# Optimization experiments

Measured on AMD Instinct MI355X. Metric: run time of the kernel, lower is better.

The kernel has to match this reference:

```python
import jax, jax.numpy as jnp
import numpy as np

# Model config (matches init_kwargs)
DIM = 2048
INTER = 1408          # moe_inter_dim
E = 16                # n_routed_experts
TOPK = 4              # n_activated_experts
G = 4                 # n_expert_groups
TOPK_G = 2            # n_limited_groups
N_SHARED = 2
SHARED_INTER = N_SHARED * INTER  # 2816
ROUTE_SCALE = 1.0


def setup_inputs() -> dict:
    key = jax.random.key(0)
    ks = jax.random.split(key, 8)
    s = 0.02
    x = jax.random.normal(ks[0], (1, 2048, DIM), dtype=jnp.float32)
    Wg = jax.random.normal(ks[1], (E, DIM), dtype=jnp.float32) * s      # gate weight
    W1 = jax.random.normal(ks[2], (E, INTER, DIM), dtype=jnp.float32) * s  # expert gate proj
    W3 = jax.random.normal(ks[3], (E, INTER, DIM), dtype=jnp.float32) * s  # expert up proj
    W2 = jax.random.normal(ks[4], (E, DIM, INTER), dtype=jnp.float32) * s  # expert down proj
    Ws1 = jax.random.normal(ks[5], (SHARED_INTER, DIM), dtype=jnp.float32) * s
    Ws3 = jax.random.normal(ks[6], (SHARED_INTER, DIM), dtype=jnp.float32) * s
    Ws2 = jax.random.normal(ks[7], (DIM, SHARED_INTER), dtype=jnp.float32) * s
    return {"x": x, "Wg": Wg, "W1": W1, "W3": W3, "W2": W2,
            "Ws1": Ws1, "Ws3": Ws3, "Ws2": Ws2}


def _moe_forward(x, Wg, W1, W3, W2, Ws1, Ws3, Ws2):
    B, S, D = x.shape
    xt = x.reshape(-1, D)              # [T, D]
    T = xt.shape[0]

    # ---- Gate: group-limited top-k routing (bias is None since dim != 7168) ----
    scores = jax.nn.softmax(xt @ Wg.T, axis=-1)          # [T, E]
    sg = scores.reshape(T, G, E // G)                    # [T, G, E/G]
    group_scores = sg.max(axis=-1)                       # amax per group
    gidx = jax.lax.top_k(group_scores, TOPK_G)[1]        # [T, TOPK_G]
    gmask = jax.nn.one_hot(gidx, G, dtype=jnp.float32).sum(axis=1) > 0  # [T, G] kept groups
    masked = jnp.where(gmask[:, :, None], sg, -jnp.inf).reshape(T, E)
    topi = jax.lax.top_k(masked, TOPK)[1]                # [T, TOPK] expert indices
    weights = jnp.take_along_axis(scores, topi, axis=1) * ROUTE_SCALE  # original_scores gather

    # ---- Routed experts: dense per-expert SwiGLU FFN, zero-weight combine ----
    # combine[t, e] = sum over k of weights[t, k] * (topi[t, k] == e)
    combine = jnp.zeros((T, E), xt.dtype).at[jnp.arange(T)[:, None], topi].add(weights)
    h = jax.nn.silu(jnp.einsum('td,eid->eti', xt, W1)) * jnp.einsum('td,eid->eti', xt, W3)
    expert_out = jnp.einsum('eti,edi->etd', h, W2)       # [E, T, D]
    y = jnp.einsum('etd,te->td', expert_out, combine)    # [T, D]

    # ---- Shared expert (applied to all tokens) ----
    z = (jax.nn.silu(xt @ Ws1.T) * (xt @ Ws3.T)) @ Ws2.T

    return (y + z).reshape(B, S, D)


def reference(x, Wg, W1, W3, W2, Ws1, Ws3, Ws2):
    return _moe_forward(x, Wg, W1, W3, W2, Ws1, Ws3, Ws2)
```

## Files before the change

kernel.cpp:

```cpp
#include <hip/hip_runtime.h>
#include <stdint.h>

#define D_MODEL  2048
#define N_INTER  1408
#define SH_INTER 2816
#define T_TOK    2048
#define NSLOT    (T_TOK * 4)
#define MIB(x)   ((size_t)(x) << 20)

typedef __attribute__((ext_vector_type(8))) short bf16x8;
typedef __attribute__((ext_vector_type(4))) float f32x4;

__device__ __forceinline__ unsigned short f2bf(float f){
  unsigned int b = __builtin_bit_cast(unsigned int, f);
  b = (b + 0x7FFFu + ((b >> 16) & 1u)) >> 16;
  return (unsigned short)b;
}
__device__ __forceinline__ float bf2f(unsigned short h){
  unsigned int b = ((unsigned int)h) << 16;
  return __builtin_bit_cast(float, b);
}

#define GLOAD16(gp, lp) __builtin_amdgcn_global_load_lds( \
    (const __attribute__((address_space(1))) unsigned int*)(gp), \
    (__attribute__((address_space(3))) unsigned int*)(lp), 16, 0, 0)

__global__ void cvt_bf16_kernel(const float* __restrict__ x,
                                unsigned short* __restrict__ o, int n4){
  const int stride = gridDim.x * blockDim.x;
  for (int i = blockIdx.x * blockDim.x + threadIdx.x; i < n4; i += stride){
    const float4 v = ((const float4*)x)[i];
    ushort4 u; u.x = f2bf(v.x); u.y = f2bf(v.y); u.z = f2bf(v.z); u.w = f2bf(v.w);
    ((ushort4*)o)[i] = u;
  }
}

__global__ void gate_kernel(const float* __restrict__ x, const float* __restrict__ Wg,
                            int* __restrict__ cnt, int* __restrict__ list,
                            float* __restrict__ wslot){
  const int t = blockIdx.x;
  const int l = threadIdx.x;
  const int e = l & 15, q = l >> 4;
  const float* xr = x + (size_t)t * D_MODEL + q * 512;
  const float* wr = Wg + (size_t)e * D_MODEL + q * 512;
  float p = 0.f;
  #pragma unroll 4
  for (int i = 0; i < 512; i += 4){
    float4 xv = *(const float4*)(xr + i);
    float4 wv = *(const float4*)(wr + i);
    p += xv.x*wv.x + xv.y*wv.y + xv.z*wv.z + xv.w*wv.w;
  }
  p += __shfl_xor(p, 16);
  p += __shfl_xor(p, 32);
  float mx = p;
  for (int d = 1; d < 16; d <<= 1) mx = fmaxf(mx, __shfl_xor(mx, d));
  float ex = __expf(p - mx);
  float sum = ex;
  for (int d = 1; d < 16; d <<= 1) sum += __shfl_xor(sum, d);
  const float sc = ex / sum;
  float gm = fmaxf(sc, __shfl_xor(sc, 1));
  gm = fmaxf(gm, __shfl_xor(gm, 2));
  const float g0 = __shfl(gm, 0), g1 = __shfl(gm, 4),
              g2 = __shfl(gm, 8), g3 = __shfl(gm, 12);
  const int grp = e >> 2;
  const float gs[4] = {g0, g1, g2, g3};
  int grank = 0;
  #pragma unroll
  for (int j = 0; j < 4; ++j)
    if (gs[j] > gm || (gs[j] == gm && j < grp)) grank++;
  const float msc = (grank < 2) ? sc : -INFINITY;
  int erank = 0;
  #pragma unroll
  for (int j = 0; j < 16; ++j){
    const float oj = __shfl(msc, j);
    if (oj > msc || (oj == msc && j < e)) erank++;
  }
  if (q == 0 && erank < 4 && msc > -INFINITY){
    const int pos = atomicAdd(&cnt[e], 1);
    const int slot = (t << 2) | erank;
    list[e * T_TOK + pos] = slot;
    wslot[slot] = sc;
  }
}

template<int GATHER>
__global__ __launch_bounds__(256, 2)
void gemm_gu2_kernel(const unsigned short* __restrict__ A,
                     const unsigned short* __restrict__ BG,
                     const unsigned short* __restrict__ BU,
                     unsigned short* __restrict__ H,
                     const int* __restrict__ list,
                     const int* __restrict__ cnt,
                     int K, int NI, int MT, int NT)
{
  __shared__ unsigned short As [3 * 4096];
  __shared__ unsigned short BsG[3 * 4096];
  __shared__ unsigned short BsU[3 * 4096];

  const int per = gridDim.x >> 3;
  const int gsw = (blockIdx.x & 7) * per + (blockIdx.x >> 3);
  const int mt   = gsw % MT;
  const int rest = gsw / MT;
  const int nt = GATHER ? (rest % NT) : rest;
  const int e  = GATHER ? (rest / NT) : 0;
  const int cntE = GATHER ? cnt[e] : (MT * 128);
  if (mt * 128 >= cntE) return;

  const int tid = threadIdx.x, wid = tid >> 6, lane = tid & 63;
  const int sx = ((lane & 3) ^ ((lane >> 3) & 3)) << 3;

  const int rt0 = 32 * wid + (lane >> 2), rt1 = rt0 + 16;
  int ar0, ar1;
  if (GATHER){
    const int lim = cntE - 1;
    int p0 = mt * 128 + rt0; p0 = p0 < lim ? p0 : lim;
    int p1 = mt * 128 + rt1; p1 = p1 < lim ? p1 : lim;
    ar0 = list[e * T_TOK + p0] >> 2;
    ar1 = list[e * T_TOK + p1] >> 2;
  } else { ar0 = mt * 128 + rt0; ar1 = mt * 128 + rt1; }
  const unsigned short* pa0 = A + (size_t)ar0 * K + sx;
  const unsigned short* pa1 = A + (size_t)ar1 * K + sx;

  const size_t eoff = GATHER ? (size_t)e * NI * K : 0;
  const unsigned short* pg0 = BG + eoff + (size_t)(nt * 128 + rt0) * K + sx;
  const unsigned short* pg1 = pg0 + (size_t)16 * K;
  const unsigned short* pu0 = BU + eoff + (size_t)(nt * 128 + rt0) * K + sx;
  const unsigned short* pu1 = pu0 + (size_t)16 * K;

  const int w0 = (32 * wid) * 32, w1 = w0 + 512;
  const int bufStr = 4096;

  const int wr = wid >> 1, wc = wid & 1, lr = lane & 15, lq = lane >> 4;
  const int fx = ((lq ^ ((lr >> 1) & 3)) << 3);
  int aoff[4], boff[4];
  #pragma unroll
  for (int m = 0; m < 4; ++m) aoff[m] = (wr * 64 + m * 16 + lr) * 32 + fx;
  #pragma unroll
  for (int n = 0; n < 4; ++n) boff[n] = (wc * 64 + n * 16 + lr) * 32 + fx;

  f32x4 accg[4][4], accu[4][4];
  const f32x4 zero = {0.f, 0.f, 0.f, 0.f};
  #pragma unroll
  for (int m = 0; m < 4; ++m)
    #pragma unroll
    for (int n = 0; n < 4; ++n){ accg[m][n] = zero; accu[m][n] = zero; }

  const int KT = K >> 5;
  #pragma unroll
  for (int t = 0; t < 3; ++t){
    GLOAD16(pa0, As  + t * bufStr + w0);
    GLOAD16(pa1, As  + t * bufStr + w1);
    GLOAD16(pg0, BsG + t * bufStr + w0);
    GLOAD16(pg1, BsG + t * bufStr + w1);
    GLOAD16(pu0, BsU + t * bufStr + w0);
    GLOAD16(pu1, BsU + t * bufStr + w1);
    pa0 += 32; pa1 += 32; pg0 += 32; pg1 += 32; pu0 += 32; pu1 += 32;
  }
  int c = 0;

  for (int kt = 0; kt < KT; ++kt){
    if (kt < KT - 2)       asm volatile("s_waitcnt vmcnt(12)" ::: "memory");
    else if (kt == KT - 2) asm volatile("s_waitcnt vmcnt(6)"  ::: "memory");
    else                   asm volatile("s_waitcnt vmcnt(0)"  ::: "memory");
    __builtin_amdgcn_s_barrier();

    const unsigned short* aC = As  + c * bufStr;
    const unsigned short* gC = BsG + c * bufStr;
    const unsigned short* uC = BsU + c * bufStr;
    bf16x8 af[4], bg[4], bu[4];
    #pragma unroll
    for (int m = 0; m < 4; ++m) af[m] = *(const bf16x8*)(aC + aoff[m]);
    #pragma unroll
    for (int n = 0; n < 4; ++n) bg[n] = *(const bf16x8*)(gC + boff[n]);
    #pragma unroll
    for (int n = 0; n < 4; ++n) bu[n] = *(const bf16x8*)(uC + boff[n]);

    asm volatile("s_waitcnt lgkmcnt(0)" ::: "memory");
    __builtin_amdgcn_sched_barrier(0);
    __builtin_amdgcn_s_barrier();

    if (kt + 3 < KT){
      GLOAD16(pa0, As  + c * bufStr + w0);
      GLOAD16(pa1, As  + c * bufStr + w1);
      GLOAD16(pg0, BsG + c * bufStr + w0);
      GLOAD16(pg1, BsG + c * bufStr + w1);
      GLOAD16(pu0, BsU + c * bufStr + w0);
      GLOAD16(pu1, BsU + c * bufStr + w1);
      pa0 += 32; pa1 += 32; pg0 += 32; pg1 += 32; pu0 += 32; pu1 += 32;
    }

    __builtin_amdgcn_s_setprio(1);
    #pragma unroll
    for (int n = 0; n < 4; ++n)
      #pragma unroll
      for (int m = 0; m < 4; ++m){
        accg[m][n] = __builtin_amdgcn_mfma_f32_16x16x32_bf16(af[m], bg[n], accg[m][n], 0, 0, 0);
        accu[m][n] = __builtin_amdgcn_mfma_f32_16x16x32_bf16(af[m], bu[n], accu[m][n], 0, 0, 0);
      }
    __builtin_amdgcn_s_setprio(0);

    c = (c == 2) ? 0 : c + 1;
  }

  const int colBase = nt * 128 + wc * 64;
  #pragma unroll
  for (int m = 0; m < 4; ++m){
    #pragma unroll
    for (int r = 0; r < 4; ++r){
      const int grow = mt * 128 + wr * 64 + m * 16 + lq * 4 + r;
      if (GATHER && grow >= cntE) continue;
      const int orow = GATHER ? list[e * T_TOK + grow] : grow;
      unsigned short* op = H + (size_t)orow * NI + colBase;
      #pragma unroll
      for (int n = 0; n < 4; ++n){
        const float g = accg[m][n][r], u = accu[m][n][r];
        op[n * 16 + lr] = f2bf(g / (1.f + __expf(-g)) * u);
      }
    }
  }
}

template<int GATHER, int KS>
__global__ __launch_bounds__(256, 2)
void gemm_down_kernel(const unsigned short* __restrict__ A,
                      const unsigned short* __restrict__ B,
                      void* __restrict__ OutP,
                      const int* __restrict__ list,
                      const int* __restrict__ cnt,
                      int K, int N, int MT, int NT)
{
  __shared__ __align__(128) char smem[24576 + 49152];
  unsigned short* As = (unsigned short*)smem;
  unsigned short* Bs = (unsigned short*)(smem + 24576);

  const int per = gridDim.x >> 3;
  const int gsw = (blockIdx.x & 7) * per + (blockIdx.x >> 3);
  const int mt   = gsw % MT;
  int rest = gsw / MT;
  const int nt = rest % NT; rest /= NT;
  const int ks = (KS > 1) ? (rest % KS) : 0;
  const int e  = GATHER ? (rest / (KS > 1 ? KS : 1)) : 0;
  const int cntE = GATHER ? cnt[e] : (MT * 128);
  if (mt * 128 >= cntE) return;

  const int tid = threadIdx.x, wid = tid >> 6, lane = tid & 63;
  const int sx = ((lane & 3) ^ ((lane >> 3) & 3)) << 3;
  const int kOff = ks * (K / KS);

  const int rt0 = 32 * wid + (lane >> 2), rt1 = rt0 + 16;
  int ar0, ar1;
  if (GATHER){
    const int lim = cntE - 1;
    int p0 = mt * 128 + rt0; p0 = p0 < lim ? p0 : lim;
    int p1 = mt * 128 + rt1; p1 = p1 < lim ? p1 : lim;
    ar0 = list[e * T_TOK + p0];
    ar1 = list[e * T_TOK + p1];
  } else { ar0 = mt * 128 + rt0; ar1 = mt * 128 + rt1; }
  const unsigned short* pa0 = A + (size_t)ar0 * K + kOff + sx;
  const unsigned short* pa1 = A + (size_t)ar1 * K + kOff + sx;

  const unsigned short* wsrc = B + (GATHER ? (size_t)e * N * K : 0) + kOff;
  const int rb = 64 * wid + (lane >> 2);
  const unsigned short* pb0 = wsrc + (size_t)(nt * 256 + rb     ) * K + sx;
  const unsigned short* pb1 = wsrc + (size_t)(nt * 256 + rb + 16) * K + sx;
  const unsigned short* pb2 = wsrc + (size_t)(nt * 256 + rb + 32) * K + sx;
  const unsigned short* pb3 = wsrc + (size_t)(nt * 256 + rb + 48) * K + sx;

  const int aW0 = (32 * wid) * 32, aW1 = aW0 + 512;
  const int bW  = (64 * wid) * 32;
  const int aStr = 128 * 32, bStr = 256 * 32;

  const int wr = wid >> 1, wc = wid & 1, lr = lane & 15, lq = lane >> 4;
  const int fx = ((lq ^ ((lr >> 1) & 3)) << 3);
  int aoff[4], boff[8];
  #pragma unroll
  for (int m = 0; m < 4; ++m) aoff[m] = (wr * 64 + m * 16 + lr) * 32 + fx;
  #pragma unroll
  for (int n = 0; n < 8; ++n) boff[n] = (wc * 128 + n * 16 + lr) * 32 + fx;

  f32x4 acc[4][8];
  const f32x4 zero = {0.f, 0.f, 0.f, 0.f};
  #pragma unroll
  for (int m = 0; m < 4; ++m)
    #pragma unroll
    for (int n = 0; n < 8; ++n) acc[m][n] = zero;

  const int KT = (K / KS) >> 5;
  #pragma unroll
  for (int t = 0; t < 3; ++t){
    GLOAD16(pa0, As + t * aStr + aW0);
    GLOAD16(pa1, As + t * aStr + aW1);
    GLOAD16(pb0, Bs + t * bStr + bW);
    GLOAD16(pb1, Bs + t * bStr + bW + 512);
    GLOAD16(pb2, Bs + t * bStr + bW + 1024);
    GLOAD16(pb3, Bs + t * bStr + bW + 1536);
    pa0 += 32; pa1 += 32; pb0 += 32; pb1 += 32; pb2 += 32; pb3 += 32;
  }
  int c = 0;

  for (int kt = 0; kt < KT; ++kt){
    if (kt < KT - 2)       asm volatile("s_waitcnt vmcnt(12)" ::: "memory");
    else if (kt == KT - 2) asm volatile("s_waitcnt vmcnt(6)"  ::: "memory");
    else                   asm volatile("s_waitcnt vmcnt(0)"  ::: "memory");
    __builtin_amdgcn_s_barrier();

    const unsigned short* aC = As + c * aStr;
    const unsigned short* bC = Bs + c * bStr;
    bf16x8 af[4], bf[8];
    #pragma unroll
    for (int m = 0; m < 4; ++m) af[m] = *(const bf16x8*)(aC + aoff[m]);
    #pragma unroll
    for (int n = 0; n < 8; ++n) bf[n] = *(const bf16x8*)(bC + boff[n]);

    asm volatile("s_waitcnt lgkmcnt(0)" ::: "memory");
    __builtin_amdgcn_sched_barrier(0);
    __builtin_amdgcn_s_barrier();

    if (kt + 3 < KT){
      GLOAD16(pa0, As + c * aStr + aW0);
      GLOAD16(pa1, As + c * aStr + aW1);
      GLOAD16(pb0, Bs + c * bStr + bW);
      GLOAD16(pb1, Bs + c * bStr + bW + 512);
      GLOAD16(pb2, Bs + c * bStr + bW + 1024);
      GLOAD16(pb3, Bs + c * bStr + bW + 1536);
      pa0 += 32; pa1 += 32; pb0 += 32; pb1 += 32; pb2 += 32; pb3 += 32;
    }

    __builtin_amdgcn_s_setprio(1);
    #pragma unroll
    for (int n = 0; n < 8; ++n)
      #pragma unroll
      for (int m = 0; m < 4; ++m)
        acc[m][n] = __builtin_amdgcn_mfma_f32_16x16x32_bf16(af[m], bf[n], acc[m][n], 0, 0, 0);
    __builtin_amdgcn_s_setprio(0);

    c = (c == 2) ? 0 : c + 1;
  }

  const int colBase = nt * 256 + wc * 128;
  #pragma unroll
  for (int m = 0; m < 4; ++m){
    #pragma unroll
    for (int r = 0; r < 4; ++r){
      const int grow = mt * 128 + wr * 64 + m * 16 + lq * 4 + r;
      if (GATHER == 0){
        float* op = (float*)OutP + (size_t)ks * MT * 128 * N + (size_t)grow * N + colBase;
        #pragma unroll
        for (int n = 0; n < 8; ++n) op[n * 16 + lr] = acc[m][n][r];
      } else {
        if (grow >= cntE) continue;
        const int orow = list[e * T_TOK + grow];
        unsigned short* op = (unsigned short*)OutP + (size_t)orow * N + colBase;
        #pragma unroll
        for (int n = 0; n < 8; ++n) op[n * 16 + lr] = f2bf(acc[m][n][r]);
      }
    }
  }
}

__global__ void combine_kernel(const unsigned short* __restrict__ H2,
                               const float* __restrict__ P,
                               const float* __restrict__ wslot,
                               float* __restrict__ out){
  const int t = blockIdx.x;
  const int ccol = threadIdx.x * 8;
  float w[4];
  #pragma unroll
  for (int k = 0; k < 4; ++k) w[k] = wslot[t * 4 + k];
  float a[8];
  #pragma unroll
  for (int j = 0; j < 8; ++j) a[j] = 0.f;
  #pragma unroll
  for (int p = 0; p < 4; ++p){
    const float* pp = P + (size_t)(p * T_TOK + t) * D_MODEL + ccol;
    #pragma unroll
    for (int j = 0; j < 8; ++j) a[j] += pp[j];
  }
  #pragma unroll
  for (int k = 0; k < 4; ++k){
    const bf16x8 hv = *(const bf16x8*)(H2 + (size_t)(t * 4 + k) * D_MODEL + ccol);
    #pragma unroll
    for (int j = 0; j < 8; ++j) a[j] += w[k] * bf2f((unsigned short)hv[j]);
  }
  float* o = out + (size_t)t * D_MODEL + ccol;
  #pragma unroll
  for (int j = 0; j < 8; ++j) o[j] = a[j];
}

extern "C" void kernel_launch(void* const* d_in, const int* in_sizes, int n_in,
                              void* d_out, int out_size, void* d_ws, size_t ws_size,
                              hipStream_t stream)
{
  const float* x   = (const float*)d_in[0];
  const float* Wg  = (const float*)d_in[1];
  const float* W1  = (const float*)d_in[2];
  const float* W3  = (const float*)d_in[3];
  const float* W2  = (const float*)d_in[4];
  const float* Ws1 = (const float*)d_in[5];
  const float* Ws3 = (const float*)d_in[6];
  const float* Ws2 = (const float*)d_in[7];
  float* out = (float*)d_out;

  char* ws = (char*)d_ws;
  int*   cnt   = (int*)(ws);
  int*   list  = (int*)(ws + 4096);
  float* wslot = (float*)(ws + 4096 + 131072);
  unsigned short* xbf = (unsigned short*)(ws + MIB(1));
  unsigned short* H2  = (unsigned short*)(ws + MIB(1));
  unsigned short* Hs  = (unsigned short*)(ws + MIB(34));
  unsigned short* Hr  = (unsigned short*)(ws + MIB(46));
  float*          P   = (float*)        (ws + MIB(70));
  unsigned short* WA  = (unsigned short*)(ws + MIB(138));
  unsigned short* WB  = (unsigned short*)(ws + MIB(231));

  hipMemsetAsync(cnt, 0, 4096, stream);
  cvt_bf16_kernel<<<2048, 256, 0, stream>>>(x, xbf, T_TOK * D_MODEL / 4);
  gate_kernel<<<T_TOK, 64, 0, stream>>>(x, Wg, cnt, list, wslot);

  cvt_bf16_kernel<<<2048, 256, 0, stream>>>(Ws1, WA, SH_INTER * D_MODEL / 4);
  cvt_bf16_kernel<<<2048, 256, 0, stream>>>(Ws3, WB, SH_INTER * D_MODEL / 4);
  gemm_gu2_kernel<0><<<16 * 22, 256, 0, stream>>>(xbf, WA, WB, Hs, nullptr, nullptr,
                                                  D_MODEL, SH_INTER, 16, 22);
  cvt_bf16_kernel<<<2048, 256, 0, stream>>>(Ws2, WA, D_MODEL * SH_INTER / 4);
  gemm_down_kernel<0, 4><<<16 * 8 * 4, 256, 0, stream>>>(Hs, WA, P, nullptr, nullptr,
                                                         SH_INTER, D_MODEL, 16, 8);

  cvt_bf16_kernel<<<8192, 256, 0, stream>>>(W1, WA, 16 * N_INTER * D_MODEL / 4);
  cvt_bf16_kernel<<<8192, 256, 0, stream>>>(W3, WB, 16 * N_INTER * D_MODEL / 4);
  gemm_gu2_kernel<1><<<16 * 11 * 16, 256, 0, stream>>>(xbf, WA, WB, Hr, list, cnt,
                                                       D_MODEL, N_INTER, 16, 11);
  cvt_bf16_kernel<<<8192, 256, 0, stream>>>(W2, WA, 16 * D_MODEL * N_INTER / 4);
  gemm_down_kernel<1, 1><<<16 * 8 * 16, 256, 0, stream>>>(Hr, WA, H2, list, cnt,
                                                          N_INTER, D_MODEL, 16, 8);
  combine_kernel<<<T_TOK, 256, 0, stream>>>(H2, P, wslot, out);
}
```

Baseline: 613.1 us.

## Overlap weight bf16 conversion with GEMMs via extra tail blocks

Routed-expert weight conversions (W1, W3, W2) are folded into the preceding GEMM launches as extra blocks, so conversion streams while the GEMM blocks compute. The four small conversions (x and the shared-expert weights) merge into one kernel. The shared down-projection drops its split-K, writes straight into the output, and combine accumulates onto it instead of summing four partial buffers. This cuts launch count and serial conversion time, but the shared down GEMM now launches only 128 GEMM blocks and competes with conversion blocks for bandwidth.

```diff
diff --git a/kernel.cpp b/kernel.cpp
--- a/kernel.cpp
+++ b/kernel.cpp
@@ -25,13 +25,36 @@
     (const __attribute__((address_space(1))) unsigned int*)(gp), \
     (__attribute__((address_space(3))) unsigned int*)(lp), 16, 0, 0)
 
-__global__ void cvt_bf16_kernel(const float* __restrict__ x,
-                                unsigned short* __restrict__ o, int n4){
+__device__ __forceinline__ void cvt_tail(const float* __restrict__ src,
+                                         unsigned short* __restrict__ dst,
+                                         int n4, int cb, int nblk, int tid){
+  const float4* s = (const float4*)src;
+  ushort4* d = (ushort4*)dst;
+  const int stride = nblk * 256;
+  for (int i = cb * 256 + tid; i < n4; i += stride){
+    const float4 v = s[i];
+    ushort4 u; u.x = f2bf(v.x); u.y = f2bf(v.y); u.z = f2bf(v.z); u.w = f2bf(v.w);
+    d[i] = u;
+  }
+}
+
+__global__ void cvt4_kernel(const float* __restrict__ x,  const float* __restrict__ Ws1,
+                            const float* __restrict__ Ws3, const float* __restrict__ Ws2,
+                            unsigned short* __restrict__ xbf, unsigned short* __restrict__ S1,
+                            unsigned short* __restrict__ S3,  unsigned short* __restrict__ S2){
+  const int N0 = T_TOK * D_MODEL / 4;
+  const int NW = SH_INTER * D_MODEL / 4;
+  const int total = N0 + 3 * NW;
   const int stride = gridDim.x * blockDim.x;
-  for (int i = blockIdx.x * blockDim.x + threadIdx.x; i < n4; i += stride){
-    const float4 v = ((const float4*)x)[i];
+  for (int i = blockIdx.x * blockDim.x + threadIdx.x; i < total; i += stride){
+    const float4* s; ushort4* d; int j;
+    if (i < N0)            { s = (const float4*)x;   d = (ushort4*)xbf; j = i; }
+    else if (i < N0 + NW)  { s = (const float4*)Ws1; d = (ushort4*)S1;  j = i - N0; }
+    else if (i < N0 + 2*NW){ s = (const float4*)Ws3; d = (ushort4*)S3;  j = i - N0 - NW; }
+    else                   { s = (const float4*)Ws2; d = (ushort4*)S2;  j = i - N0 - 2*NW; }
+    const float4 v = s[j];
     ushort4 u; u.x = f2bf(v.x); u.y = f2bf(v.y); u.z = f2bf(v.z); u.w = f2bf(v.w);
-    ((ushort4*)o)[i] = u;
+    d[j] = u;
   }
 }
 
@@ -91,14 +114,24 @@
                      unsigned short* __restrict__ H,
                      const int* __restrict__ list,
                      const int* __restrict__ cnt,
-                     int K, int NI, int MT, int NT)
+                     int K, int NI, int MT, int NT,
+                     const float* __restrict__ cvtSrc,
+                     unsigned short* __restrict__ cvtDst,
+                     int cvtN4, int gemmN)
 {
   __shared__ unsigned short As [3 * 4096];
   __shared__ unsigned short BsG[3 * 4096];
   __shared__ unsigned short BsU[3 * 4096];
 
-  const int per = gridDim.x >> 3;
-  const int gsw = (blockIdx.x & 7) * per + (blockIdx.x >> 3);
+  const int tid = threadIdx.x;
+  const int bid = blockIdx.x;
+  if (bid >= gemmN){
+    cvt_tail(cvtSrc, cvtDst, cvtN4, bid - gemmN, gridDim.x - gemmN, tid);
+    return;
+  }
+
+  const int per = gemmN >> 3;
+  const int gsw = (bid & 7) * per + (bid >> 3);
   const int mt   = gsw % MT;
   const int rest = gsw / MT;
   const int nt = GATHER ? (rest % NT) : rest;
@@ -106,7 +139,7 @@
   const int cntE = GATHER ? cnt[e] : (MT * 128);
   if (mt * 128 >= cntE) return;
 
-  const int tid = threadIdx.x, wid = tid >> 6, lane = tid & 63;
+  const int wid = tid >> 6, lane = tid & 63;
   const int sx = ((lane & 3) ^ ((lane >> 3) & 3)) << 3;
 
   const int rt0 = 32 * wid + (lane >> 2), rt1 = rt0 + 16;
@@ -220,32 +253,40 @@
   }
 }
 
-template<int GATHER, int KS>
+template<int GATHER>
 __global__ __launch_bounds__(256, 2)
 void gemm_down_kernel(const unsigned short* __restrict__ A,
                       const unsigned short* __restrict__ B,
                       void* __restrict__ OutP,
                       const int* __restrict__ list,
                       const int* __restrict__ cnt,
-                      int K, int N, int MT, int NT)
+                      int K, int N, int MT, int NT,
+                      const float* __restrict__ cvtSrc,
+                      unsigned short* __restrict__ cvtDst,
+                      int cvtN4, int gemmN)
 {
   __shared__ __align__(128) char smem[24576 + 49152];
   unsigned short* As = (unsigned short*)smem;
   unsigned short* Bs = (unsigned short*)(smem + 24576);
 
-  const int per = gridDim.x >> 3;
-  const int gsw = (blockIdx.x & 7) * per + (blockIdx.x >> 3);
+  const int tid = threadIdx.x;
+  const int bid = blockIdx.x;
+  if (bid >= gemmN){
+    cvt_tail(cvtSrc, cvtDst, cvtN4, bid - gemmN, gridDim.x - gemmN, tid);
+    return;
+  }
+
+  const int per = gemmN >> 3;
+  const int gsw = (bid & 7) * per + (bid >> 3);
   const int mt   = gsw % MT;
-  int rest = gsw / MT;
-  const int nt = rest % NT; rest /= NT;
-  const int ks = (KS > 1) ? (rest % KS) : 0;
-  const int e  = GATHER ? (rest / (KS > 1 ? KS : 1)) : 0;
+  const int rest = gsw / MT;
+  const int nt = rest % NT;
+  const int e  = GATHER ? (rest / NT) : 0;
   const int cntE = GATHER ? cnt[e] : (MT * 128);
   if (mt * 128 >= cntE) return;
 
-  const int tid = threadIdx.x, wid = tid >> 6, lane = tid & 63;
+  const int wid = tid >> 6, lane = tid & 63;
   const int sx = ((lane & 3) ^ ((lane >> 3) & 3)) << 3;
-  const int kOff = ks * (K / KS);
 
   const int rt0 = 32 * wid + (lane >> 2), rt1 = rt0 + 16;
   int ar0, ar1;
@@ -256,10 +297,10 @@
     ar0 = list[e * T_TOK + p0];
     ar1 = list[e * T_TOK + p1];
   } else { ar0 = mt * 128 + rt0; ar1 = mt * 128 + rt1; }
-  const unsigned short* pa0 = A + (size_t)ar0 * K + kOff + sx;
-  const unsigned short* pa1 = A + (size_t)ar1 * K + kOff + sx;
-
-  const unsigned short* wsrc = B + (GATHER ? (size_t)e * N * K : 0) + kOff;
+  const unsigned short* pa0 = A + (size_t)ar0 * K + sx;
+  const unsigned short* pa1 = A + (size_t)ar1 * K + sx;
+
+  const unsigned short* wsrc = B + (GATHER ? (size_t)e * N * K : 0);
   const int rb = 64 * wid + (lane >> 2);
   const unsigned short* pb0 = wsrc + (size_t)(nt * 256 + rb     ) * K + sx;
   const unsigned short* pb1 = wsrc + (size_t)(nt * 256 + rb + 16) * K + sx;
@@ -285,7 +326,7 @@
     #pragma unroll
     for (int n = 0; n < 8; ++n) acc[m][n] = zero;
 
-  const int KT = (K / KS) >> 5;
+  const int KT = K >> 5;
   #pragma unroll
   for (int t = 0; t < 3; ++t){
     GLOAD16(pa0, As + t * aStr + aW0);
@@ -344,7 +385,7 @@
     for (int r = 0; r < 4; ++r){
       const int grow = mt * 128 + wr * 64 + m * 16 + lq * 4 + r;
       if (GATHER == 0){
-        float* op = (float*)OutP + (size_t)ks * MT * 128 * N + (size_t)grow * N + colBase;
+        float* op = (float*)OutP + (size_t)grow * N + colBase;
         #pragma unroll
         for (int n = 0; n < 8; ++n) op[n * 16 + lr] = acc[m][n][r];
       } else {
@@ -359,7 +400,6 @@
 }
 
 __global__ void combine_kernel(const unsigned short* __restrict__ H2,
-                               const float* __restrict__ P,
                                const float* __restrict__ wslot,
                                float* __restrict__ out){
   const int t = blockIdx.x;
@@ -367,22 +407,16 @@
   float w[4];
   #pragma unroll
   for (int k = 0; k < 4; ++k) w[k] = wslot[t * 4 + k];
+  float* o = out + (size_t)t * D_MODEL + ccol;
   float a[8];
   #pragma unroll
-  for (int j = 0; j < 8; ++j) a[j] = 0.f;
-  #pragma unroll
-  for (int p = 0; p < 4; ++p){
-    const float* pp = P + (size_t)(p * T_TOK + t) * D_MODEL + ccol;
-    #pragma unroll
-    for (int j = 0; j < 8; ++j) a[j] += pp[j];
-  }
+  for (int j = 0; j < 8; ++j) a[j] = o[j];
   #pragma unroll
   for (int k = 0; k < 4; ++k){
     const bf16x8 hv = *(const bf16x8*)(H2 + (size_t)(t * 4 + k) * D_MODEL + ccol);
     #pragma unroll
     for (int j = 0; j < 8; ++j) a[j] += w[k] * bf2f((unsigned short)hv[j]);
   }
-  float* o = out + (size_t)t * D_MODEL + ccol;
   #pragma unroll
   for (int j = 0; j < 8; ++j) o[j] = a[j];
 }
@@ -406,31 +440,37 @@
   int*   list  = (int*)(ws + 4096);
   float* wslot = (float*)(ws + 4096 + 131072);
   unsigned short* xbf = (unsigned short*)(ws + MIB(1));
-  unsigned short* H2  = (unsigned short*)(ws + MIB(1));
-  unsigned short* Hs  = (unsigned short*)(ws + MIB(34));
-  unsigned short* Hr  = (unsigned short*)(ws + MIB(46));
-  float*          P   = (float*)        (ws + MIB(70));
-  unsigned short* WA  = (unsigned short*)(ws + MIB(138));
-  unsigned short* WB  = (unsigned short*)(ws + MIB(231));
+  unsigned short* S1  = (unsigned short*)(ws + MIB(9));
+  unsigned short* S3  = (unsigned short*)(ws + MIB(21));
+  unsigned short* S2  = (unsigned short*)(ws + MIB(33));
+  unsigned short* Hs  = (unsigned short*)(ws + MIB(45));
+  unsigned short* Hr  = (unsigned short*)(ws + MIB(57));
+  unsigned short* H2  = (unsigned short*)(ws + MIB(80));
+  unsigned short* W1b = (unsigned short*)(ws + MIB(112));
+  unsigned short* W3b = (unsigned short*)(ws + MIB(204));
+  unsigned short* W2b = (unsigned short*)(ws + MIB(296));
+
+  const int NW_R = 16 * N_INTER * D_MODEL / 4;
 
   hipMemsetAsync(cnt, 0, 4096, stream);
-  cvt_bf16_kernel<<<2048, 256, 0, stream>>>(x, xbf, T_TOK * D_MODEL / 4);
+  cvt4_kernel<<<2048, 256, 0, stream>>>(x, Ws1, Ws3, Ws2, xbf, S1, S3, S2);
   gate_kernel<<<T_TOK, 64, 0, stream>>>(x, Wg, cnt, list, wslot);
 
-  cvt_bf16_kernel<<<2048, 256, 0, stream>>>(Ws1, WA, SH_INTER * D_MODEL / 4);
-  cvt_bf16_kernel<<<2048, 256, 0, stream>>>(Ws3, WB, SH_INTER * D_MODEL / 4);
-  gemm_gu2_kernel<0><<<16 * 22, 256, 0, stream>>>(xbf, WA, WB, Hs, nullptr, nullptr,
-                                                  D_MODEL, SH_INTER, 16, 22);
-  cvt_bf16_kernel<<<2048, 256, 0, stream>>>(Ws2, WA, D_MODEL * SH_INTER / 4);
-  gemm_down_kernel<0, 4><<<16 * 8 * 4, 256, 0, stream>>>(Hs, WA, P, nullptr, nullptr,
-                                                         SH_INTER, D_MODEL, 16, 8);
-
-  cvt_bf16_kernel<<<8192, 256, 0, stream>>>(W1, WA, 16 * N_INTER * D_MODEL / 4);
-  cvt_bf16_kernel<<<8192, 256, 0, stream>>>(W3, WB, 16 * N_INTER * D_MODEL / 4);
-  gemm_gu2_kernel<1><<<16 * 11 * 16, 256, 0, stream>>>(xbf, WA, WB, Hr, list, cnt,
-                                                       D_MODEL, N_INTER, 16, 11);
-  cvt_bf16_kernel<<<8192, 256, 0, stream>>>(W2, WA, 16 * D_MODEL * N_INTER / 4);
-  gemm_down_kernel<1, 1><<<16 * 8 * 16, 256, 0, stream>>>(Hr, WA, H2, list, cnt,
-                                                          N_INTER, D_MODEL, 16, 8);
-  combine_kernel<<<T_TOK, 256, 0, stream>>>(H2, P, wslot, out);
-}
+  gemm_gu2_kernel<0><<<352 + 1600, 256, 0, stream>>>(
+      xbf, S1, S3, Hs, nullptr, nullptr, D_MODEL, SH_INTER, 16, 22,
+      W1, W1b, NW_R, 352);
+
+  gemm_down_kernel<0><<<128 + 1664, 256, 0, stream>>>(
+      Hs, S2, out, nullptr, nullptr, SH_INTER, D_MODEL, 16, 8,
+      W3, W3b, NW_R, 128);
+
+  gemm_gu2_kernel<1><<<2816 + 1280, 256, 0, stream>>>(
+      xbf, W1b, W3b, Hr, list, cnt, D_MODEL, N_INTER, 16, 11,
+      W2, W2b, NW_R, 2816);
+
+  gemm_down_kernel<1><<<2048, 256, 0, stream>>>(
+      Hr, W2b, H2, list, cnt, N_INTER, D_MODEL, 16, 8,
+      nullptr, nullptr, 0, 2048);
+
+  combine_kernel<<<T_TOK, 256, 0, stream>>>(H2, wslot, out);
+}
```

Measured after the change: 626.5 us. 2.2% more time.
